# Kernel tuning notes

Measured on AMD Instinct MI355X. Metric: run time of the kernel, lower is better.

## Reference

```python
import jax, jax.numpy as jnp
import numpy as np

ALPHA = 0.2          # LeakyReLU negative slope
NEG_BIG = -9e15      # zero_vec value used before softmax masking


def setup_inputs() -> dict:
    key = jax.random.key(0)
    k1, k2, k3, k4, k5 = jax.random.split(key, 5)
    N, M, F, K = 2048, 8192, 1024, 10
    feature_matrix = jax.random.normal(k1, (N, F), dtype=jnp.float32)
    embed_matrix = jax.random.normal(k2, (M, F), dtype=jnp.float32)
    # Xavier-ish scaling for params
    weight = jax.random.normal(k3, (F, F), dtype=jnp.float32) * (1.0 / np.sqrt(F))
    a = jax.random.normal(k4, (2 * F, 1), dtype=jnp.float32) * (1.0 / np.sqrt(2 * F))
    neigh_idx = jax.random.randint(k5, (N, K), 0, M, dtype=jnp.int64)
    return {
        "feature_matrix": feature_matrix,
        "embed_matrix": embed_matrix,
        "weight": weight,
        "a": a,
        "neigh_idx": neigh_idx,
    }


def reference(feature_matrix, embed_matrix, weight, a, neigh_idx):
    # feature_matrix: [N, F] features of batch nodes
    # embed_matrix:   [M, F] features of unique sampled neighbors
    # neigh_idx:      [N, K] sampled neighbor columns (set semantics: dups collapse)
    N, F = feature_matrix.shape
    M = embed_matrix.shape[0]
    rows = jnp.arange(N)[:, None]
    mask = jnp.zeros((N, M), dtype=feature_matrix.dtype).at[rows, neigh_idx].set(1.0)

    # GAT kernel path
    hf = feature_matrix @ weight          # [N, F]
    he = embed_matrix @ weight            # [M, F]
    # e_ij = leakyrelu([h_i || h_j] . a) == leakyrelu(h_i.a1 + h_j.a2)
    a1 = a[:F, 0]
    a2 = a[F:, 0]
    e = (hf @ a1)[:, None] + (he @ a2)[None, :]          # [N, M]
    e = jnp.where(e > 0, e, ALPHA * e)                   # LeakyReLU(0.2)
    scores = jnp.where(mask > 0, e, NEG_BIG)
    attention = jax.nn.softmax(scores, axis=1)           # row softmax
    to_feats = attention @ he                            # [N, F]
    return to_feats
```

## Files before the change

kernel.cpp:

```cpp
#include <hip/hip_runtime.h>
#include <math.h>

#define ALPHA 0.2f
#define MAXK 10

typedef _Float16 half8 __attribute__((ext_vector_type(8)));
typedef _Float16 half4 __attribute__((ext_vector_type(4)));
typedef float f32x4 __attribute__((ext_vector_type(4)));

__device__ __forceinline__ void gload_lds16(const void* g, void* l) {
    __builtin_amdgcn_global_load_lds(
        (const __attribute__((address_space(1))) unsigned int*)g,
        (__attribute__((address_space(3))) unsigned int*)l, 16, 0, 0);
}

__global__ void wa_kernel(const float* __restrict__ W, const float* __restrict__ a,
                          float* __restrict__ wa, int F) {
    int wave = (int)((blockIdx.x * blockDim.x + threadIdx.x) >> 6);
    int lane = threadIdx.x & 63;
    if (wave >= F) return;
    const float4* wr = reinterpret_cast<const float4*>(W + (size_t)wave * F);
    const float4* a1 = reinterpret_cast<const float4*>(a);
    const float4* a2 = reinterpret_cast<const float4*>(a + F);
    float acc1 = 0.f, acc2 = 0.f;
    int F4 = F >> 2;
    for (int c = lane; c < F4; c += 64) {
        float4 w = wr[c];
        float4 x = a1[c];
        float4 y = a2[c];
        acc1 += w.x * x.x + w.y * x.y + w.z * x.z + w.w * x.w;
        acc2 += w.x * y.x + w.y * y.y + w.z * y.z + w.w * y.w;
    }
    #pragma unroll
    for (int off = 32; off; off >>= 1) {
        acc1 += __shfl_down(acc1, off);
        acc2 += __shfl_down(acc2, off);
    }
    if (lane == 0) { wa[wave] = acc1; wa[F + wave] = acc2; }
}

__global__ __launch_bounds__(256) void mid_kernel(
    const float* __restrict__ feat, const float* __restrict__ embed,
    const int* __restrict__ nidx, const float* __restrict__ wa,
    const float* __restrict__ W, _Float16* __restrict__ agg,
    _Float16* __restrict__ Wt, int F, int N) {
    const int tid = threadIdx.x;

    if ((int)blockIdx.x >= N) {
        __shared__ float t[32][33];
        const int tb = blockIdx.x - N;
        const int tpr = F >> 5;
        const int bx = (tb % tpr) * 32;
        const int by = (tb / tpr) * 32;
        const int x = tid & 31, y = tid >> 5;
        for (int i = y; i < 32; i += 8)
            t[i][x] = W[(size_t)(bx + i) * F + by + x];
        __syncthreads();
        for (int i = y; i < 32; i += 8)
            Wt[(size_t)(by + i) * F + bx + x] = (_Float16)t[x][i];
        return;
    }

    const int i = blockIdx.x;
    const int f = tid * 4;

    int idx[MAXK];
    bool dup[MAXK];
    #pragma unroll
    for (int k = 0; k < MAXK; k++) idx[k] = nidx[i * MAXK + k];
    #pragma unroll
    for (int k = 0; k < MAXK; k++) {
        bool d = false;
        #pragma unroll
        for (int p = 0; p < MAXK; p++)
            if (p < k) d |= (idx[p] == idx[k]);
        dup[k] = d;
    }

    float4 wa1 = *(const float4*)&wa[f];
    float4 wa2 = *(const float4*)&wa[F + f];
    float4 fv  = *(const float4*)&feat[(size_t)i * F + f];
    float a1p = fv.x * wa1.x + fv.y * wa1.y + fv.z * wa1.z + fv.w * wa1.w;

    float4 rv[MAXK];
    float a2p[MAXK];
    #pragma unroll
    for (int k = 0; k < MAXK; k++) {
        rv[k] = *(const float4*)&embed[(size_t)idx[k] * F + f];
        a2p[k] = rv[k].x * wa2.x + rv[k].y * wa2.y + rv[k].z * wa2.z + rv[k].w * wa2.w;
    }

    #pragma unroll
    for (int off = 32; off; off >>= 1) {
        a1p += __shfl_down(a1p, off);
        #pragma unroll
        for (int k = 0; k < MAXK; k++) a2p[k] += __shfl_down(a2p[k], off);
    }
    __shared__ float red[MAXK + 1][4];
    const int w = tid >> 6, l = tid & 63;
    if (l == 0) {
        red[0][w] = a1p;
        #pragma unroll
        for (int k = 0; k < MAXK; k++) red[k + 1][w] = a2p[k];
    }
    __syncthreads();

    float s1 = red[0][0] + red[0][1] + red[0][2] + red[0][3];
    float sc[MAXK];
    float m = -INFINITY;
    #pragma unroll
    for (int k = 0; k < MAXK; k++) {
        float v = s1 + red[k + 1][0] + red[k + 1][1] + red[k + 1][2] + red[k + 1][3];
        v = v > 0.f ? v : ALPHA * v;
        sc[k] = v;
        if (!dup[k]) m = fmaxf(m, v);
    }
    float sum = 0.f;
    #pragma unroll
    for (int k = 0; k < MAXK; k++) {
        sc[k] = dup[k] ? 0.f : expf(sc[k] - m);
        sum += sc[k];
    }
    float inv = 1.0f / sum;

    float4 o = make_float4(0.f, 0.f, 0.f, 0.f);
    #pragma unroll
    for (int k = 0; k < MAXK; k++) {
        float wk = sc[k] * inv;
        o.x += wk * rv[k].x;
        o.y += wk * rv[k].y;
        o.z += wk * rv[k].z;
        o.w += wk * rv[k].w;
    }
    half4 h = { (_Float16)o.x, (_Float16)o.y, (_Float16)o.z, (_Float16)o.w };
    *(half4*)&agg[(size_t)i * F + f] = h;
}

__global__ __launch_bounds__(256) void gemm_f16_kernel(
    const _Float16* __restrict__ A, const _Float16* __restrict__ Bt,
    float* __restrict__ C, int M, int N, int K) {
    __shared__ _Float16 As[2][64 * 64];
    __shared__ _Float16 Bs[2][64 * 64];
    const int tid = threadIdx.x;

    int bid = blockIdx.y * gridDim.x + blockIdx.x;
    int nwg = gridDim.x * gridDim.y;
    int cpx = nwg >> 3;
    int wg = (bid & 7) * cpx + (bid >> 3);
    const int m0 = (wg / gridDim.x) * 64;
    const int n0 = (wg % gridDim.x) * 64;

    const int l = tid & 63, wv = tid >> 6;
    const int wm = wv >> 1, wn = wv & 1;
    const int lrow = l & 15, kc = l >> 4;

    const int srow = l >> 3;
    const int sslot = (l & 7) ^ (srow & 7);
    const int nt = K >> 6;

    f32x4 acc[2][2] = {};

    const int rg0 = wv * 2, rg1 = wv * 2 + 1;

    #define STAGE(buf, t)                                                          \
    do {                                                                           \
        int k0_ = (t) * 64;                                                        \
        gload_lds16(&A[(size_t)(m0 + rg0 * 8 + srow) * K + k0_ + sslot * 8],       \
                    (void*)((char*)&As[buf][0] + rg0 * 1024 + l * 16));            \
        gload_lds16(&A[(size_t)(m0 + rg1 * 8 + srow) * K + k0_ + sslot * 8],       \
                    (void*)((char*)&As[buf][0] + rg1 * 1024 + l * 16));            \
        gload_lds16(&Bt[(size_t)(n0 + rg0 * 8 + srow) * K + k0_ + sslot * 8],      \
                    (void*)((char*)&Bs[buf][0] + rg0 * 1024 + l * 16));            \
        gload_lds16(&Bt[(size_t)(n0 + rg1 * 8 + srow) * K + k0_ + sslot * 8],      \
                    (void*)((char*)&Bs[buf][0] + rg1 * 1024 + l * 16));            \
    } while (0)

    STAGE(0, 0);
    asm volatile("s_waitcnt vmcnt(0)" ::: "memory");
    __syncthreads();

    int buf = 0;
    for (int t = 0; t < nt; ++t) {
        if (t + 1 < nt) STAGE(buf ^ 1, t + 1);

        half8 av[2][2], bv[2][2];
        #pragma unroll
        for (int ks = 0; ks < 2; ks++) {
            #pragma unroll
            for (int fq = 0; fq < 2; fq++) {
                int arow = wm * 32 + fq * 16 + lrow;
                int aslot = (ks * 4 + kc) ^ (arow & 7);
                av[ks][fq] = *(const half8*)((const char*)&As[buf][0] + arow * 128 + aslot * 16);
                int brow = wn * 32 + fq * 16 + lrow;
                int bslot = (ks * 4 + kc) ^ (brow & 7);
                bv[ks][fq] = *(const half8*)((const char*)&Bs[buf][0] + brow * 128 + bslot * 16);
            }
        }
        #pragma unroll
        for (int ks = 0; ks < 2; ks++)
            #pragma unroll
            for (int fq = 0; fq < 2; fq++)
                #pragma unroll
                for (int g = 0; g < 2; g++)
                    acc[fq][g] = __builtin_amdgcn_mfma_f32_16x16x32_f16(
                        av[ks][fq], bv[ks][g], acc[fq][g], 0, 0, 0);

        asm volatile("s_waitcnt vmcnt(0)" ::: "memory");
        __syncthreads();
        buf ^= 1;
    }
    #undef STAGE

    #pragma unroll
    for (int fq = 0; fq < 2; fq++)
        #pragma unroll
        for (int g = 0; g < 2; g++)
            #pragma unroll
            for (int r = 0; r < 4; r++)
                C[(size_t)(m0 + wm * 32 + fq * 16 + kc * 4 + r) * N
                  + n0 + wn * 32 + g * 16 + lrow] = acc[fq][g][r];
}

extern "C" void kernel_launch(void* const* d_in, const int* in_sizes, int n_in,
                              void* d_out, int out_size, void* d_ws, size_t ws_size,
                              hipStream_t stream) {
    const float* feat  = (const float*)d_in[0];
    const float* embed = (const float*)d_in[1];
    const float* W     = (const float*)d_in[2];
    const float* a     = (const float*)d_in[3];
    const int*   nidx  = (const int*)d_in[4];

    int F = in_sizes[3] / 2;
    int N = in_sizes[0] / F;
    int M = in_sizes[1] / F;

    float* ws = (float*)d_ws;
    float* wa = ws;
    _Float16* agg_f16 = (_Float16*)(wa + 2 * F);
    _Float16* wt_f16  = agg_f16 + (size_t)N * F;
    (void)M;

    wa_kernel<<<(F * 64 + 255) / 256, 256, 0, stream>>>(W, a, wa, F);
    {
        int tblocks = (F / 32) * (F / 32);
        mid_kernel<<<N + tblocks, 256, 0, stream>>>(feat, embed, nidx, wa, W,
                                                    agg_f16, wt_f16, F, N);
    }
    {
        dim3 grid(F / 64, N / 64);
        gemm_f16_kernel<<<grid, 256, 0, stream>>>(agg_f16, wt_f16, (float*)d_out, N, F, F);
    }
}
```

Baseline: 37.66 us.

## Double K tile to 128 and overlap prefetch with partial vmcnt waits

```diff
diff --git a/kernel.cpp b/kernel.cpp
--- a/kernel.cpp
+++ b/kernel.cpp
@@ -139,8 +139,8 @@
 __global__ __launch_bounds__(256) void gemm_f16_kernel(
     const _Float16* __restrict__ A, const _Float16* __restrict__ Bt,
     float* __restrict__ C, int M, int N, int K) {
-    __shared__ _Float16 As[2][64 * 64];
-    __shared__ _Float16 Bs[2][64 * 64];
+    __shared__ _Float16 As[2][64 * 128];
+    __shared__ _Float16 Bs[2][64 * 128];
     const int tid = threadIdx.x;
 
     int bid = blockIdx.y * gridDim.x + blockIdx.x;
@@ -153,60 +153,66 @@
     const int l = tid & 63, wv = tid >> 6;
     const int wm = wv >> 1, wn = wv & 1;
     const int lrow = l & 15, kc = l >> 4;
-
-    const int srow = l >> 3;
-    const int sslot = (l & 7) ^ (srow & 7);
-    const int nt = K >> 6;
+    const int nt = K >> 7;
 
     f32x4 acc[2][2] = {};
 
-    const int rg0 = wv * 2, rg1 = wv * 2 + 1;
-
-    #define STAGE(buf, t)                                                          \
-    do {                                                                           \
-        int k0_ = (t) * 64;                                                        \
-        gload_lds16(&A[(size_t)(m0 + rg0 * 8 + srow) * K + k0_ + sslot * 8],       \
-                    (void*)((char*)&As[buf][0] + rg0 * 1024 + l * 16));            \
-        gload_lds16(&A[(size_t)(m0 + rg1 * 8 + srow) * K + k0_ + sslot * 8],       \
-                    (void*)((char*)&As[buf][0] + rg1 * 1024 + l * 16));            \
-        gload_lds16(&Bt[(size_t)(n0 + rg0 * 8 + srow) * K + k0_ + sslot * 8],      \
-                    (void*)((char*)&Bs[buf][0] + rg0 * 1024 + l * 16));            \
-        gload_lds16(&Bt[(size_t)(n0 + rg1 * 8 + srow) * K + k0_ + sslot * 8],      \
-                    (void*)((char*)&Bs[buf][0] + rg1 * 1024 + l * 16));            \
+    #define STAGE(bf, t)                                                            \
+    do {                                                                            \
+        int k0_ = (t) * 128;                                                        \
+        _Pragma("unroll")                                                           \
+        for (int j_ = 0; j_ < 4; j_++) {                                            \
+            int u_ = wv * 256 + j_ * 64 + l;                                        \
+            int row_ = u_ >> 4, slot_ = (u_ & 15) ^ (row_ & 7);                     \
+            gload_lds16(&A[(size_t)(m0 + row_) * K + k0_ + slot_ * 8],              \
+                        (void*)((char*)&As[bf][0] + u_ * 16));                      \
+        }                                                                           \
+        _Pragma("unroll")                                                           \
+        for (int j_ = 0; j_ < 4; j_++) {                                            \
+            int u_ = wv * 256 + j_ * 64 + l;                                        \
+            int row_ = u_ >> 4, slot_ = (u_ & 15) ^ (row_ & 7);                     \
+            gload_lds16(&Bt[(size_t)(n0 + row_) * K + k0_ + slot_ * 8],             \
+                        (void*)((char*)&Bs[bf][0] + u_ * 16));                      \
+        }                                                                           \
     } while (0)
 
     STAGE(0, 0);
-    asm volatile("s_waitcnt vmcnt(0)" ::: "memory");
-    __syncthreads();
 
     int buf = 0;
     for (int t = 0; t < nt; ++t) {
-        if (t + 1 < nt) STAGE(buf ^ 1, t + 1);
-
-        half8 av[2][2], bv[2][2];
-        #pragma unroll
-        for (int ks = 0; ks < 2; ks++) {
+        if (t + 1 < nt) {
+            STAGE(buf ^ 1, t + 1);
+            asm volatile("s_waitcnt vmcnt(8)" ::: "memory");
+        } else {
+            asm volatile("s_waitcnt vmcnt(0)" ::: "memory");
+        }
+        __builtin_amdgcn_s_barrier();
+        __builtin_amdgcn_sched_barrier(0);
+
+        __builtin_amdgcn_s_setprio(1);
+        #pragma unroll
+        for (int ks = 0; ks < 4; ks++) {
+            half8 av[2], bv[2];
             #pragma unroll
             for (int fq = 0; fq < 2; fq++) {
                 int arow = wm * 32 + fq * 16 + lrow;
-                int aslot = (ks * 4 + kc) ^ (arow & 7);
-                av[ks][fq] = *(const half8*)((const char*)&As[buf][0] + arow * 128 + aslot * 16);
+                int ag = (ks * 4 + kc) ^ (arow & 7);
+                av[fq] = *(const half8*)((const char*)&As[buf][0] + arow * 256 + ag * 16);
                 int brow = wn * 32 + fq * 16 + lrow;
-                int bslot = (ks * 4 + kc) ^ (brow & 7);
-                bv[ks][fq] = *(const half8*)((const char*)&Bs[buf][0] + brow * 128 + bslot * 16);
+                int bg = (ks * 4 + kc) ^ (brow & 7);
+                bv[fq] = *(const half8*)((const char*)&Bs[buf][0] + brow * 256 + bg * 16);
             }
-        }
-        #pragma unroll
-        for (int ks = 0; ks < 2; ks++)
             #pragma unroll
             for (int fq = 0; fq < 2; fq++)
                 #pragma unroll
                 for (int g = 0; g < 2; g++)
                     acc[fq][g] = __builtin_amdgcn_mfma_f32_16x16x32_f16(
-                        av[ks][fq], bv[ks][g], acc[fq][g], 0, 0, 0);
-
-        asm volatile("s_waitcnt vmcnt(0)" ::: "memory");
-        __syncthreads();
+                        av[fq], bv[g], acc[fq][g], 0, 0, 0);
+        }
+        __builtin_amdgcn_s_setprio(0);
+
+        __builtin_amdgcn_sched_barrier(0);
+        __builtin_amdgcn_s_barrier();
         buf ^= 1;
     }
     #undef STAGE
```

Measured after the change: 36.79 us. 2.3% less time.
